# Optimization experiments

Measured on AMD Instinct MI355X. Metric: run time of the kernel, lower is better.

The kernel has to match this reference:

```python
import jax, jax.numpy as jnp
import numpy as np
import itertools

# Fixed 3x5 signal matrix from the module
_M = jnp.array([[1., 0., 0., 0., 0.],
                [0., 0., 1., 1., -1.],
                [0., 1., 0., -1., 1.]], dtype=jnp.float32)
# All 6 permutations of 3 elements (itertools order, matching torch code)
_PERM = jnp.array(list(itertools.permutations(range(3))), dtype=jnp.int32)  # [6,3]

B, DIN, G = 8192, 3072, 1024  # dout = 3*G = 3072


def setup_inputs() -> dict:
    key = jax.random.key(0)
    k1, k2, k3, k4 = jax.random.split(key, 4)
    x = jax.random.normal(k1, (B, DIN), dtype=jnp.float32)
    connections = jax.random.randint(k2, (G, 3), 0, DIN)  # int indices into din
    selector = jax.random.normal(k3, (G, 3), dtype=jnp.float32)
    wgts = jax.random.normal(k4, (G, 6), dtype=jnp.float32)
    return {"x": x, "connections": connections, "selector": selector, "wgts": wgts}


def reference(x, connections, selector, wgts):
    # 1. gather 3 inputs per gate: [B, G, 3]
    inputs = jnp.take(x, connections, axis=1)
    # 2. soft selector blend (training path)
    C = selector / (1.0 + jnp.abs(selector))           # [G, 3]
    absC = jnp.abs(C)
    gated = (1.0 - absC)[None] * inputs + ((C + absC) * 0.5)[None]  # [B, G, 3]
    # 3-4. all 6 permutations of the 3 gate inputs: [B, G, 6, 3]
    p = gated[:, :, _PERM]
    # 5. interaction columns -> [B, G, 6, 5]
    feat = jnp.concatenate([
        p,
        (p[..., 0] * p[..., 1])[..., None],
        (p[..., 0] * p[..., 2])[..., None],
    ], axis=-1)
    # 6-7. Signals = M @ feat^T over last dims: [B, G, 3, 6]
    signals = jnp.einsum('ms,bgps->bgmp', _M, feat)
    # 8. softmax-weighted sum over the 6 permutations: [B, G, 3]
    w = jax.nn.softmax(wgts, axis=1)                   # [G, 6]
    out = jnp.einsum('bgmp,gp->bgm', signals, w)
    # 10. flatten to [B, 3*G] = [B, dout]
    return out.reshape(out.shape[0], -1)
```

## Files before the change

kernel.cpp:

```cpp
#include <hip/hip_runtime.h>

#define G_ 1024
#define DIN_ 3072
#define B_ 8192
#define TB 4

__global__ __launch_bounds__(256) void fredkin_coef_kernel(
    const int* __restrict__ conn, const float* __restrict__ sel,
    const float* __restrict__ wg, float* __restrict__ coef)
{
    int g = blockIdx.x * blockDim.x + threadIdx.x;
    if (g >= G_) return;

    float u[3], v[3];
#pragma unroll
    for (int i = 0; i < 3; ++i) {
        float s = sel[g * 3 + i];
        float C = s / (1.0f + fabsf(s));
        float a = fabsf(C);
        u[i] = 1.0f - a;
        v[i] = 0.5f * (C + a);
    }

    float w[6];
    float mx = -1e30f;
#pragma unroll
    for (int p = 0; p < 6; ++p) mx = fmaxf(mx, wg[g * 6 + p]);
    float sum = 0.0f;
#pragma unroll
    for (int p = 0; p < 6; ++p) { w[p] = expf(wg[g * 6 + p] - mx); sum += w[p]; }
    float inv = 1.0f / sum;
#pragma unroll
    for (int p = 0; p < 6; ++p) w[p] *= inv;

    const int P[6][3] = {{0,1,2},{0,2,1},{1,0,2},{1,2,0},{2,0,1},{2,1,0}};
    float L[3][3] = {{0.f,0.f,0.f},{0.f,0.f,0.f},{0.f,0.f,0.f}};
    float Q[3][3] = {{0.f,0.f,0.f},{0.f,0.f,0.f},{0.f,0.f,0.f}};
#pragma unroll
    for (int p = 0; p < 6; ++p) {
        int i0 = P[p][0], i1 = P[p][1], i2 = P[p][2];
        float wp = w[p];
        int p01 = i0 + i1 - 1;
        int p02 = i0 + i2 - 1;
        L[0][i0] += wp;
        L[1][i2] += wp; Q[1][p01] += wp; Q[1][p02] -= wp;
        L[2][i1] += wp; Q[2][p01] -= wp; Q[2][p02] += wp;
    }

#pragma unroll
    for (int m = 0; m < 3; ++m) {
        float K = L[m][0]*v[0] + L[m][1]*v[1] + L[m][2]*v[2]
                + Q[m][0]*v[0]*v[1] + Q[m][1]*v[0]*v[2] + Q[m][2]*v[1]*v[2];
        float cx0 = u[0]*(L[m][0] + Q[m][0]*v[1] + Q[m][1]*v[2]);
        float cx1 = u[1]*(L[m][1] + Q[m][0]*v[0] + Q[m][2]*v[2]);
        float cx2 = u[2]*(L[m][2] + Q[m][1]*v[0] + Q[m][2]*v[1]);
        float cq01 = Q[m][0]*u[0]*u[1];
        float cq02 = Q[m][1]*u[0]*u[2];
        float cq12 = Q[m][2]*u[1]*u[2];
        float* o = coef + (size_t)g * 24 + m * 8;
        o[0]=K; o[1]=cx0; o[2]=cx1; o[3]=cx2; o[4]=cq01; o[5]=cq02; o[6]=cq12; o[7]=0.f;
    }
}

__global__ __launch_bounds__(256) void fredkin_main_kernel(
    const float* __restrict__ x, const int* __restrict__ conn,
    const float* __restrict__ coef, float* __restrict__ out)
{
    __shared__ float xs[TB * DIN_];
    const int t = threadIdx.x;
    const int row0 = blockIdx.x * TB;

    const float4* xv = (const float4*)(x + (size_t)row0 * DIN_);
    float4* sv = (float4*)xs;
#pragma unroll
    for (int i = 0; i < (TB * DIN_ / 4) / 256; ++i)
        sv[t + i * 256] = xv[t + i * 256];
    __syncthreads();

    for (int gi = 0; gi < G_ / 256; ++gi) {
        const int g = t + gi * 256;
        const int c0 = conn[g * 3 + 0];
        const int c1 = conn[g * 3 + 1];
        const int c2 = conn[g * 3 + 2];
        const float4* cf = (const float4*)(coef + (size_t)g * 24);
        const float4 a0 = cf[0], q0 = cf[1];
        const float4 a1 = cf[2], q1 = cf[3];
        const float4 a2 = cf[4], q2 = cf[5];
#pragma unroll
        for (int r = 0; r < TB; ++r) {
            const float x0 = xs[r * DIN_ + c0];
            const float x1 = xs[r * DIN_ + c1];
            const float x2 = xs[r * DIN_ + c2];
            const float p01 = x0 * x1, p02 = x0 * x2, p12 = x1 * x2;
            float o0 = a0.x + a0.y*x0 + a0.z*x1 + a0.w*x2 + q0.x*p01 + q0.y*p02 + q0.z*p12;
            float o1 = a1.x + a1.y*x0 + a1.z*x1 + a1.w*x2 + q1.x*p01 + q1.y*p02 + q1.z*p12;
            float o2 = a2.x + a2.y*x0 + a2.z*x1 + a2.w*x2 + q2.x*p01 + q2.y*p02 + q2.z*p12;
            const size_t off = (size_t)(row0 + r) * (3 * G_) + 3 * g;
            out[off + 0] = o0;
            out[off + 1] = o1;
            out[off + 2] = o2;
        }
    }
}

extern "C" void kernel_launch(void* const* d_in, const int* in_sizes, int n_in,
                              void* d_out, int out_size, void* d_ws, size_t ws_size,
                              hipStream_t stream) {
    const float* x    = (const float*)d_in[0];
    const int*   conn = (const int*)d_in[1];
    const float* sel  = (const float*)d_in[2];
    const float* wg   = (const float*)d_in[3];
    float* out  = (float*)d_out;
    float* coef = (float*)d_ws;

    hipLaunchKernelGGL(fredkin_coef_kernel, dim3(G_ / 256), dim3(256), 0, stream,
                       conn, sel, wg, coef);
    hipLaunchKernelGGL(fredkin_main_kernel, dim3(B_ / TB), dim3(256), 0, stream,
                       x, conn, coef, out);
}
```

Baseline: 41.59 us.

## Use 1024-thread blocks with one gate per thread and packed conn+coef records

The main kernel now launches 1024 threads per block, so each thread handles exactly one gate and loads its connection indices and coefficients once, from a single packed 128-byte record that the coef kernel writes. The separate conn load is gone, and each thread issues all shared-memory gathers before doing the arithmetic. The goal is more memory-level parallelism and fewer per-gate global loads. In exchange, the larger blocks may lower occupancy given the 48KB of LDS each block uses, and the workspace record grows to 32 floats per gate.

Result: slower. 48.64 us (+17.0%).

```diff
diff --git a/kernel.cpp b/kernel.cpp
--- a/kernel.cpp
+++ b/kernel.cpp
@@ -4,10 +4,11 @@
 #define DIN_ 3072
 #define B_ 8192
 #define TB 4
+#define TPB 1024
 
 __global__ __launch_bounds__(256) void fredkin_coef_kernel(
     const int* __restrict__ conn, const float* __restrict__ sel,
-    const float* __restrict__ wg, float* __restrict__ coef)
+    const float* __restrict__ wg, float* __restrict__ cw)
 {
     int g = blockIdx.x * blockDim.x + threadIdx.x;
     if (g >= G_) return;
@@ -47,6 +48,13 @@
         L[2][i1] += wp; Q[2][p01] -= wp; Q[2][p02] += wp;
     }
 
+    float* o = cw + (size_t)g * 32;
+    int* oi = (int*)o;
+    oi[0] = conn[g * 3 + 0];
+    oi[1] = conn[g * 3 + 1];
+    oi[2] = conn[g * 3 + 2];
+    oi[3] = 0;
+
 #pragma unroll
     for (int m = 0; m < 3; ++m) {
         float K = L[m][0]*v[0] + L[m][1]*v[1] + L[m][2]*v[2]
@@ -54,52 +62,53 @@
         float cx0 = u[0]*(L[m][0] + Q[m][0]*v[1] + Q[m][1]*v[2]);
         float cx1 = u[1]*(L[m][1] + Q[m][0]*v[0] + Q[m][2]*v[2]);
         float cx2 = u[2]*(L[m][2] + Q[m][1]*v[0] + Q[m][2]*v[1]);
-        float cq01 = Q[m][0]*u[0]*u[1];
-        float cq02 = Q[m][1]*u[0]*u[2];
-        float cq12 = Q[m][2]*u[1]*u[2];
-        float* o = coef + (size_t)g * 24 + m * 8;
-        o[0]=K; o[1]=cx0; o[2]=cx1; o[3]=cx2; o[4]=cq01; o[5]=cq02; o[6]=cq12; o[7]=0.f;
+        float* om = o + 4 + m * 8;
+        om[0]=K; om[1]=cx0; om[2]=cx1; om[3]=cx2;
+        om[4]=Q[m][0]*u[0]*u[1]; om[5]=Q[m][1]*u[0]*u[2]; om[6]=Q[m][2]*u[1]*u[2];
+        om[7]=0.f;
     }
 }
 
-__global__ __launch_bounds__(256) void fredkin_main_kernel(
-    const float* __restrict__ x, const int* __restrict__ conn,
-    const float* __restrict__ coef, float* __restrict__ out)
+__global__ __launch_bounds__(1024) void fredkin_main_kernel(
+    const float* __restrict__ x, const float* __restrict__ cw,
+    float* __restrict__ out)
 {
     __shared__ float xs[TB * DIN_];
     const int t = threadIdx.x;
     const int row0 = blockIdx.x * TB;
 
+    const float4* cf = (const float4*)(cw + (size_t)t * 32);
+    const int4 cc = ((const int4*)cf)[0];
+    const float4 a0 = cf[1], q0 = cf[2];
+    const float4 a1 = cf[3], q1 = cf[4];
+    const float4 a2 = cf[5], q2 = cf[6];
+    const int c0 = cc.x, c1 = cc.y, c2 = cc.z;
+
     const float4* xv = (const float4*)(x + (size_t)row0 * DIN_);
     float4* sv = (float4*)xs;
 #pragma unroll
-    for (int i = 0; i < (TB * DIN_ / 4) / 256; ++i)
-        sv[t + i * 256] = xv[t + i * 256];
+    for (int i = 0; i < (TB * DIN_ / 4) / TPB; ++i)
+        sv[t + i * TPB] = xv[t + i * TPB];
     __syncthreads();
 
-    for (int gi = 0; gi < G_ / 256; ++gi) {
-        const int g = t + gi * 256;
-        const int c0 = conn[g * 3 + 0];
-        const int c1 = conn[g * 3 + 1];
-        const int c2 = conn[g * 3 + 2];
-        const float4* cf = (const float4*)(coef + (size_t)g * 24);
-        const float4 a0 = cf[0], q0 = cf[1];
-        const float4 a1 = cf[2], q1 = cf[3];
-        const float4 a2 = cf[4], q2 = cf[5];
+    float g0[TB], g1[TB], g2[TB];
 #pragma unroll
-        for (int r = 0; r < TB; ++r) {
-            const float x0 = xs[r * DIN_ + c0];
-            const float x1 = xs[r * DIN_ + c1];
-            const float x2 = xs[r * DIN_ + c2];
-            const float p01 = x0 * x1, p02 = x0 * x2, p12 = x1 * x2;
-            float o0 = a0.x + a0.y*x0 + a0.z*x1 + a0.w*x2 + q0.x*p01 + q0.y*p02 + q0.z*p12;
-            float o1 = a1.x + a1.y*x0 + a1.z*x1 + a1.w*x2 + q1.x*p01 + q1.y*p02 + q1.z*p12;
-            float o2 = a2.x + a2.y*x0 + a2.z*x1 + a2.w*x2 + q2.x*p01 + q2.y*p02 + q2.z*p12;
-            const size_t off = (size_t)(row0 + r) * (3 * G_) + 3 * g;
-            out[off + 0] = o0;
-            out[off + 1] = o1;
-            out[off + 2] = o2;
-        }
+    for (int r = 0; r < TB; ++r) {
+        g0[r] = xs[r * DIN_ + c0];
+        g1[r] = xs[r * DIN_ + c1];
+        g2[r] = xs[r * DIN_ + c2];
+    }
+#pragma unroll
+    for (int r = 0; r < TB; ++r) {
+        const float x0 = g0[r], x1 = g1[r], x2 = g2[r];
+        const float p01 = x0 * x1, p02 = x0 * x2, p12 = x1 * x2;
+        float o0 = a0.x + a0.y*x0 + a0.z*x1 + a0.w*x2 + q0.x*p01 + q0.y*p02 + q0.z*p12;
+        float o1 = a1.x + a1.y*x0 + a1.z*x1 + a1.w*x2 + q1.x*p01 + q1.y*p02 + q1.z*p12;
+        float o2 = a2.x + a2.y*x0 + a2.z*x1 + a2.w*x2 + q2.x*p01 + q2.y*p02 + q2.z*p12;
+        const size_t off = (size_t)(row0 + r) * (3 * G_) + 3 * t;
+        out[off + 0] = o0;
+        out[off + 1] = o1;
+        out[off + 2] = o2;
     }
 }
 
@@ -110,11 +119,11 @@
     const int*   conn = (const int*)d_in[1];
     const float* sel  = (const float*)d_in[2];
     const float* wg   = (const float*)d_in[3];
-    float* out  = (float*)d_out;
-    float* coef = (float*)d_ws;
+    float* out = (float*)d_out;
+    float* cw  = (float*)d_ws;
 
     hipLaunchKernelGGL(fredkin_coef_kernel, dim3(G_ / 256), dim3(256), 0, stream,
-                       conn, sel, wg, coef);
-    hipLaunchKernelGGL(fredkin_main_kernel, dim3(B_ / TB), dim3(256), 0, stream,
-                       x, conn, coef, out);
+                       conn, sel, wg, cw);
+    hipLaunchKernelGGL(fredkin_main_kernel, dim3(B_ / TB), dim3(TPB), 0, stream,
+                       x, cw, out);
 }
```

## Load x tiles via direct global-to-LDS loads and process two row tiles per block

Applied to the files above, without the earlier changes.

The main kernel now copies x rows into shared memory with the global_load_lds builtin, which writes straight to LDS instead of going through registers. Each block handles two 4-row tiles in sequence, with a barrier between them. Connection indices are hoisted into registers once per block, and the LDS gathers for all rows are issued before the arithmetic. This aims to cut register-staging overhead and per-block setup, at the cost of half as many blocks and less parallelism to hide latency.

New measurement: 43.04 us. 3.5% more time.

```diff
diff --git a/kernel.cpp b/kernel.cpp
--- a/kernel.cpp
+++ b/kernel.cpp
@@ -4,6 +4,8 @@
 #define DIN_ 3072
 #define B_ 8192
 #define TB 4
+#define RT 2
+#define TPB 256
 
 __global__ __launch_bounds__(256) void fredkin_coef_kernel(
     const int* __restrict__ conn, const float* __restrict__ sel,
@@ -54,51 +56,70 @@
         float cx0 = u[0]*(L[m][0] + Q[m][0]*v[1] + Q[m][1]*v[2]);
         float cx1 = u[1]*(L[m][1] + Q[m][0]*v[0] + Q[m][2]*v[2]);
         float cx2 = u[2]*(L[m][2] + Q[m][1]*v[0] + Q[m][2]*v[1]);
-        float cq01 = Q[m][0]*u[0]*u[1];
-        float cq02 = Q[m][1]*u[0]*u[2];
-        float cq12 = Q[m][2]*u[1]*u[2];
-        float* o = coef + (size_t)g * 24 + m * 8;
-        o[0]=K; o[1]=cx0; o[2]=cx1; o[3]=cx2; o[4]=cq01; o[5]=cq02; o[6]=cq12; o[7]=0.f;
+        float* om = coef + (size_t)g * 24 + m * 8;
+        om[0]=K; om[1]=cx0; om[2]=cx1; om[3]=cx2;
+        om[4]=Q[m][0]*u[0]*u[1]; om[5]=Q[m][1]*u[0]*u[2]; om[6]=Q[m][2]*u[1]*u[2];
+        om[7]=0.f;
     }
 }
 
-__global__ __launch_bounds__(256) void fredkin_main_kernel(
+__global__ __launch_bounds__(TPB) void fredkin_main_kernel(
     const float* __restrict__ x, const int* __restrict__ conn,
     const float* __restrict__ coef, float* __restrict__ out)
 {
     __shared__ float xs[TB * DIN_];
     const int t = threadIdx.x;
-    const int row0 = blockIdx.x * TB;
 
-    const float4* xv = (const float4*)(x + (size_t)row0 * DIN_);
-    float4* sv = (float4*)xs;
+    int c0[4], c1[4], c2[4];
 #pragma unroll
-    for (int i = 0; i < (TB * DIN_ / 4) / 256; ++i)
-        sv[t + i * 256] = xv[t + i * 256];
-    __syncthreads();
+    for (int gi = 0; gi < 4; ++gi) {
+        const int g = t + gi * TPB;
+        c0[gi] = conn[g * 3 + 0];
+        c1[gi] = conn[g * 3 + 1];
+        c2[gi] = conn[g * 3 + 2];
+    }
 
-    for (int gi = 0; gi < G_ / 256; ++gi) {
-        const int g = t + gi * 256;
-        const int c0 = conn[g * 3 + 0];
-        const int c1 = conn[g * 3 + 1];
-        const int c2 = conn[g * 3 + 2];
-        const float4* cf = (const float4*)(coef + (size_t)g * 24);
-        const float4 a0 = cf[0], q0 = cf[1];
-        const float4 a1 = cf[2], q1 = cf[3];
-        const float4 a2 = cf[4], q2 = cf[5];
+    for (int tile = 0; tile < RT; ++tile) {
+        const int row0 = (blockIdx.x * RT + tile) * TB;
+        if (tile) __syncthreads();
+
+        const float4* xv = (const float4*)(x + (size_t)row0 * DIN_);
+        float4* sv = (float4*)xs;
 #pragma unroll
-        for (int r = 0; r < TB; ++r) {
-            const float x0 = xs[r * DIN_ + c0];
-            const float x1 = xs[r * DIN_ + c1];
-            const float x2 = xs[r * DIN_ + c2];
-            const float p01 = x0 * x1, p02 = x0 * x2, p12 = x1 * x2;
-            float o0 = a0.x + a0.y*x0 + a0.z*x1 + a0.w*x2 + q0.x*p01 + q0.y*p02 + q0.z*p12;
-            float o1 = a1.x + a1.y*x0 + a1.z*x1 + a1.w*x2 + q1.x*p01 + q1.y*p02 + q1.z*p12;
-            float o2 = a2.x + a2.y*x0 + a2.z*x1 + a2.w*x2 + q2.x*p01 + q2.y*p02 + q2.z*p12;
-            const size_t off = (size_t)(row0 + r) * (3 * G_) + 3 * g;
-            out[off + 0] = o0;
-            out[off + 1] = o1;
-            out[off + 2] = o2;
+        for (int i = 0; i < (TB * DIN_ / 4) / TPB; ++i) {
+            __builtin_amdgcn_global_load_lds(
+                (const __attribute__((address_space(1))) void*)(xv + t + i * TPB),
+                (__attribute__((address_space(3))) void*)(sv + t + i * TPB),
+                16, 0, 0);
+        }
+        __syncthreads();
+
+#pragma unroll 2
+        for (int gi = 0; gi < 4; ++gi) {
+            const int g = t + gi * TPB;
+            const float4* cf = (const float4*)(coef + (size_t)g * 24);
+            const float4 a0 = cf[0], q0 = cf[1];
+            const float4 a1 = cf[2], q1 = cf[3];
+            const float4 a2 = cf[4], q2 = cf[5];
+            float g0[TB], g1[TB], g2[TB];
+#pragma unroll
+            for (int r = 0; r < TB; ++r) {
+                g0[r] = xs[r * DIN_ + c0[gi]];
+                g1[r] = xs[r * DIN_ + c1[gi]];
+                g2[r] = xs[r * DIN_ + c2[gi]];
+            }
+#pragma unroll
+            for (int r = 0; r < TB; ++r) {
+                const float x0 = g0[r], x1 = g1[r], x2 = g2[r];
+                const float p01 = x0 * x1, p02 = x0 * x2, p12 = x1 * x2;
+                float o0 = a0.x + a0.y*x0 + a0.z*x1 + a0.w*x2 + q0.x*p01 + q0.y*p02 + q0.z*p12;
+                float o1 = a1.x + a1.y*x0 + a1.z*x1 + a1.w*x2 + q1.x*p01 + q1.y*p02 + q1.z*p12;
+                float o2 = a2.x + a2.y*x0 + a2.z*x1 + a2.w*x2 + q2.x*p01 + q2.y*p02 + q2.z*p12;
+                const size_t off = (size_t)(row0 + r) * (3 * G_) + 3 * g;
+                out[off + 0] = o0;
+                out[off + 1] = o1;
+                out[off + 2] = o2;
+            }
         }
     }
 }
@@ -115,6 +136,6 @@
 
     hipLaunchKernelGGL(fredkin_coef_kernel, dim3(G_ / 256), dim3(256), 0, stream,
                        conn, sel, wg, coef);
-    hipLaunchKernelGGL(fredkin_main_kernel, dim3(B_ / TB), dim3(256), 0, stream,
+    hipLaunchKernelGGL(fredkin_main_kernel, dim3(B_ / (TB * RT)), dim3(TPB), 0, stream,
                        x, conn, coef, out);
 }
```

## Fuse coefficient computation into main kernel with async LDS loads and vector stores

Applied to the files above, without the earlier changes.

Drops the separate coefficient kernel. Each block now recomputes the per-gate polynomial coefficients in registers, with 512 threads handling 2 gates each, while x rows are streamed into LDS through global_load_lds so the load overlaps that arithmetic. Output goes out as float2 stores of 6 contiguous values per thread instead of scalar strided stores. The aim is to remove a launch, the coefficient round-trip through memory, and uncoalesced writes. In exchange, every block redundantly recomputes the softmax and coefficients, and register pressure rises.

Result: faster. 39.00 us (-6.2%).

```diff
diff --git a/kernel.cpp b/kernel.cpp
--- a/kernel.cpp
+++ b/kernel.cpp
@@ -4,67 +4,13 @@
 #define DIN_ 3072
 #define B_ 8192
 #define TB 4
+#define TPB 512
+#define GPT 2
 
-__global__ __launch_bounds__(256) void fredkin_coef_kernel(
-    const int* __restrict__ conn, const float* __restrict__ sel,
-    const float* __restrict__ wg, float* __restrict__ coef)
-{
-    int g = blockIdx.x * blockDim.x + threadIdx.x;
-    if (g >= G_) return;
-
-    float u[3], v[3];
-#pragma unroll
-    for (int i = 0; i < 3; ++i) {
-        float s = sel[g * 3 + i];
-        float C = s / (1.0f + fabsf(s));
-        float a = fabsf(C);
-        u[i] = 1.0f - a;
-        v[i] = 0.5f * (C + a);
-    }
-
-    float w[6];
-    float mx = -1e30f;
-#pragma unroll
-    for (int p = 0; p < 6; ++p) mx = fmaxf(mx, wg[g * 6 + p]);
-    float sum = 0.0f;
-#pragma unroll
-    for (int p = 0; p < 6; ++p) { w[p] = expf(wg[g * 6 + p] - mx); sum += w[p]; }
-    float inv = 1.0f / sum;
-#pragma unroll
-    for (int p = 0; p < 6; ++p) w[p] *= inv;
-
-    const int P[6][3] = {{0,1,2},{0,2,1},{1,0,2},{1,2,0},{2,0,1},{2,1,0}};
-    float L[3][3] = {{0.f,0.f,0.f},{0.f,0.f,0.f},{0.f,0.f,0.f}};
-    float Q[3][3] = {{0.f,0.f,0.f},{0.f,0.f,0.f},{0.f,0.f,0.f}};
-#pragma unroll
-    for (int p = 0; p < 6; ++p) {
-        int i0 = P[p][0], i1 = P[p][1], i2 = P[p][2];
-        float wp = w[p];
-        int p01 = i0 + i1 - 1;
-        int p02 = i0 + i2 - 1;
-        L[0][i0] += wp;
-        L[1][i2] += wp; Q[1][p01] += wp; Q[1][p02] -= wp;
-        L[2][i1] += wp; Q[2][p01] -= wp; Q[2][p02] += wp;
-    }
-
-#pragma unroll
-    for (int m = 0; m < 3; ++m) {
-        float K = L[m][0]*v[0] + L[m][1]*v[1] + L[m][2]*v[2]
-                + Q[m][0]*v[0]*v[1] + Q[m][1]*v[0]*v[2] + Q[m][2]*v[1]*v[2];
-        float cx0 = u[0]*(L[m][0] + Q[m][0]*v[1] + Q[m][1]*v[2]);
-        float cx1 = u[1]*(L[m][1] + Q[m][0]*v[0] + Q[m][2]*v[2]);
-        float cx2 = u[2]*(L[m][2] + Q[m][1]*v[0] + Q[m][2]*v[1]);
-        float cq01 = Q[m][0]*u[0]*u[1];
-        float cq02 = Q[m][1]*u[0]*u[2];
-        float cq12 = Q[m][2]*u[1]*u[2];
-        float* o = coef + (size_t)g * 24 + m * 8;
-        o[0]=K; o[1]=cx0; o[2]=cx1; o[3]=cx2; o[4]=cq01; o[5]=cq02; o[6]=cq12; o[7]=0.f;
-    }
-}
-
-__global__ __launch_bounds__(256) void fredkin_main_kernel(
+__global__ __launch_bounds__(TPB, 4) void fredkin_fused_kernel(
     const float* __restrict__ x, const int* __restrict__ conn,
-    const float* __restrict__ coef, float* __restrict__ out)
+    const float* __restrict__ sel, const float* __restrict__ wg,
+    float* __restrict__ out)
 {
     __shared__ float xs[TB * DIN_];
     const int t = threadIdx.x;
@@ -73,33 +19,95 @@
     const float4* xv = (const float4*)(x + (size_t)row0 * DIN_);
     float4* sv = (float4*)xs;
 #pragma unroll
-    for (int i = 0; i < (TB * DIN_ / 4) / 256; ++i)
-        sv[t + i * 256] = xv[t + i * 256];
+    for (int i = 0; i < (TB * DIN_ / 4) / TPB; ++i)
+        __builtin_amdgcn_global_load_lds(
+            (const __attribute__((address_space(1))) void*)(xv + t + i * TPB),
+            (__attribute__((address_space(3))) void*)(sv + t + i * TPB),
+            16, 0, 0);
+
+    int   cc[GPT][3];
+    float CF[GPT][3][7];
+#pragma unroll
+    for (int gi = 0; gi < GPT; ++gi) {
+        const int g = t * GPT + gi;
+
+        float u[3], v[3];
+#pragma unroll
+        for (int i = 0; i < 3; ++i) {
+            cc[gi][i] = conn[g * 3 + i];
+            float s = sel[g * 3 + i];
+            float C = s / (1.0f + fabsf(s));
+            float a = fabsf(C);
+            u[i] = 1.0f - a;
+            v[i] = 0.5f * (C + a);
+        }
+
+        float w[6];
+        float mx = -1e30f;
+#pragma unroll
+        for (int p = 0; p < 6; ++p) mx = fmaxf(mx, wg[g * 6 + p]);
+        float sum = 0.0f;
+#pragma unroll
+        for (int p = 0; p < 6; ++p) { w[p] = __expf(wg[g * 6 + p] - mx); sum += w[p]; }
+        float inv = 1.0f / sum;
+#pragma unroll
+        for (int p = 0; p < 6; ++p) w[p] *= inv;
+
+        const int P[6][3] = {{0,1,2},{0,2,1},{1,0,2},{1,2,0},{2,0,1},{2,1,0}};
+        float L[3][3] = {{0.f,0.f,0.f},{0.f,0.f,0.f},{0.f,0.f,0.f}};
+        float Q[3][3] = {{0.f,0.f,0.f},{0.f,0.f,0.f},{0.f,0.f,0.f}};
+#pragma unroll
+        for (int p = 0; p < 6; ++p) {
+            int i0 = P[p][0], i1 = P[p][1], i2 = P[p][2];
+            float wp = w[p];
+            int p01 = i0 + i1 - 1;
+            int p02 = i0 + i2 - 1;
+            L[0][i0] += wp;
+            L[1][i2] += wp; Q[1][p01] += wp; Q[1][p02] -= wp;
+            L[2][i1] += wp; Q[2][p01] -= wp; Q[2][p02] += wp;
+        }
+
+#pragma unroll
+        for (int m = 0; m < 3; ++m) {
+            CF[gi][m][0] = L[m][0]*v[0] + L[m][1]*v[1] + L[m][2]*v[2]
+                         + Q[m][0]*v[0]*v[1] + Q[m][1]*v[0]*v[2] + Q[m][2]*v[1]*v[2];
+            CF[gi][m][1] = u[0]*(L[m][0] + Q[m][0]*v[1] + Q[m][1]*v[2]);
+            CF[gi][m][2] = u[1]*(L[m][1] + Q[m][0]*v[0] + Q[m][2]*v[2]);
+            CF[gi][m][3] = u[2]*(L[m][2] + Q[m][1]*v[0] + Q[m][2]*v[1]);
+            CF[gi][m][4] = Q[m][0]*u[0]*u[1];
+            CF[gi][m][5] = Q[m][1]*u[0]*u[2];
+            CF[gi][m][6] = Q[m][2]*u[1]*u[2];
+        }
+    }
+
     __syncthreads();
 
-    for (int gi = 0; gi < G_ / 256; ++gi) {
-        const int g = t + gi * 256;
-        const int c0 = conn[g * 3 + 0];
-        const int c1 = conn[g * 3 + 1];
-        const int c2 = conn[g * 3 + 2];
-        const float4* cf = (const float4*)(coef + (size_t)g * 24);
-        const float4 a0 = cf[0], q0 = cf[1];
-        const float4 a1 = cf[2], q1 = cf[3];
-        const float4 a2 = cf[4], q2 = cf[5];
 #pragma unroll
-        for (int r = 0; r < TB; ++r) {
-            const float x0 = xs[r * DIN_ + c0];
-            const float x1 = xs[r * DIN_ + c1];
-            const float x2 = xs[r * DIN_ + c2];
+    for (int r = 0; r < TB; ++r) {
+        const float* xb = xs + r * DIN_;
+        float gx[GPT][3];
+#pragma unroll
+        for (int gi = 0; gi < GPT; ++gi) {
+            gx[gi][0] = xb[cc[gi][0]];
+            gx[gi][1] = xb[cc[gi][1]];
+            gx[gi][2] = xb[cc[gi][2]];
+        }
+        float o[GPT * 3];
+#pragma unroll
+        for (int gi = 0; gi < GPT; ++gi) {
+            const float x0 = gx[gi][0], x1 = gx[gi][1], x2 = gx[gi][2];
             const float p01 = x0 * x1, p02 = x0 * x2, p12 = x1 * x2;
-            float o0 = a0.x + a0.y*x0 + a0.z*x1 + a0.w*x2 + q0.x*p01 + q0.y*p02 + q0.z*p12;
-            float o1 = a1.x + a1.y*x0 + a1.z*x1 + a1.w*x2 + q1.x*p01 + q1.y*p02 + q1.z*p12;
-            float o2 = a2.x + a2.y*x0 + a2.z*x1 + a2.w*x2 + q2.x*p01 + q2.y*p02 + q2.z*p12;
-            const size_t off = (size_t)(row0 + r) * (3 * G_) + 3 * g;
-            out[off + 0] = o0;
-            out[off + 1] = o1;
-            out[off + 2] = o2;
+#pragma unroll
+            for (int m = 0; m < 3; ++m) {
+                o[gi * 3 + m] = CF[gi][m][0]
+                              + CF[gi][m][1]*x0 + CF[gi][m][2]*x1 + CF[gi][m][3]*x2
+                              + CF[gi][m][4]*p01 + CF[gi][m][5]*p02 + CF[gi][m][6]*p12;
+            }
         }
+        float2* op = (float2*)(out + (size_t)(row0 + r) * (3 * G_) + (size_t)t * (3 * GPT));
+        op[0] = make_float2(o[0], o[1]);
+        op[1] = make_float2(o[2], o[3]);
+        op[2] = make_float2(o[4], o[5]);
     }
 }
 
@@ -110,11 +118,8 @@
     const int*   conn = (const int*)d_in[1];
     const float* sel  = (const float*)d_in[2];
     const float* wg   = (const float*)d_in[3];
-    float* out  = (float*)d_out;
-    float* coef = (float*)d_ws;
+    float* out = (float*)d_out;
 
-    hipLaunchKernelGGL(fredkin_coef_kernel, dim3(G_ / 256), dim3(256), 0, stream,
-                       conn, sel, wg, coef);
-    hipLaunchKernelGGL(fredkin_main_kernel, dim3(B_ / TB), dim3(256), 0, stream,
-                       x, conn, coef, out);
+    hipLaunchKernelGGL(fredkin_fused_kernel, dim3(B_ / TB), dim3(TPB), 0, stream,
+                       x, conn, sel, wg, out);
 }
```
